# Kernel tuning notes

Measured on AMD Instinct MI355X. Metric: run time of the kernel, lower is better.

## Reference

```python
import jax, jax.numpy as jnp
import numpy as np

N = 20000      # nodes (B in the original code)
T = 8          # timesteps
D_IN = 256     # in_dim (must equal hid_dim due to conv_h_n reuse in original)
D_HID = 256
D_OUT = 64
E = 320000     # edges


def setup_inputs() -> dict:
    key = jax.random.key(0)
    ks = jax.random.split(key, 18)
    s = 0.05
    w = lambda k, shape: jax.random.normal(k, shape, jnp.float32) * s
    return {
        "x": jax.random.normal(ks[0], (N, T, D_IN), jnp.float32),
        "edge_index": jax.random.randint(ks[1], (2, E), 0, N),
        "W_xr": w(ks[2], (D_IN, D_HID)),  "b_xr": w(ks[3], (D_HID,)),
        "W_hr": w(ks[4], (D_HID, D_HID)), "b_hr": w(ks[5], (D_HID,)),
        "W_xz": w(ks[6], (D_IN, D_HID)),  "b_xz": w(ks[7], (D_HID,)),
        "W_hz": w(ks[8], (D_HID, D_HID)), "b_hz": w(ks[9], (D_HID,)),
        "W_hn": w(ks[10], (D_HID, D_HID)), "b_hn": w(ks[11], (D_HID,)),
        "W_fc": w(ks[12], (D_HID, D_OUT)), "b_fc": w(ks[13], (D_OUT,)),
    }


def reference(x, edge_index, W_xr, b_xr, W_hr, b_hr, W_xz, b_xz, W_hz, b_hz,
              W_hn, b_hn, W_fc, b_fc):
    n_nodes = x.shape[0]
    src, dst = edge_index[0], edge_index[1]

    # GCN symmetric normalization with self-loops (PyG GCNConv default):
    # deg[i] = 1 + #incoming edges; norm_e = d^-1/2[src]*d^-1/2[dst]
    deg = jax.ops.segment_sum(jnp.ones(src.shape[0], x.dtype), dst,
                              num_segments=n_nodes) + jnp.asarray(1.0, x.dtype)
    dis = jax.lax.rsqrt(deg)
    enorm = dis[src] * dis[dst]      # [E]
    snorm = dis * dis                # self-loop coefficient 1/deg, [N]

    def gcn(v, W, b):
        vw = v @ W                                              # [N, D]
        agg = jax.ops.segment_sum(vw[src] * enorm[:, None], dst,
                                  num_segments=n_nodes)
        return agg + vw * snorm[:, None] + b

    def step(h, x_t):
        r = jax.nn.sigmoid(gcn(x_t, W_xr, b_xr) + gcn(h, W_hr, b_hr))
        z = jax.nn.sigmoid(gcn(x_t, W_xz, b_xz) + gcn(h, W_hz, b_hz))
        # faithful to original: conv_h_n is applied to BOTH x and h
        n = jnp.tanh(gcn(x_t, W_hn, b_hn) + r * gcn(h, W_hn, b_hn))
        h_new = (1.0 - z) * h + z * n
        return h_new, None

    h0 = jnp.zeros((n_nodes, W_hr.shape[0]), x.dtype)
    h, _ = jax.lax.scan(step, h0, jnp.transpose(x, (1, 0, 2)))  # scan over T
    return h @ W_fc + b_fc
```

## Files before the change

### kernel.cpp

```cpp
#include <hip/hip_runtime.h>
#include <hip/hip_bf16.h>
#include <math.h>

#define N_NODES 20000
#define T_STEPS 8
#define DDIM    256
#define DOUT    64
#define NE      320000
#define XSTR    2048

typedef unsigned short u16;
typedef __attribute__((ext_vector_type(8))) short  short8;
typedef __attribute__((ext_vector_type(4))) float  f32x4;

__device__ __forceinline__ float bf2f(u16 u) {
    union { unsigned int i; float f; } v; v.i = ((unsigned int)u) << 16; return v.f;
}
__device__ __forceinline__ u16 f2bf(float f) {
    union { float f; unsigned int i; } v; v.f = f;
    unsigned int r = v.i + 0x7fff + ((v.i >> 16) & 1);
    return (u16)(r >> 16);
}

__global__ void k_count(const int* __restrict__ dst, int* __restrict__ cnt) {
    int e = blockIdx.x * blockDim.x + threadIdx.x;
    if (e < NE) atomicAdd(&cnt[dst[e]], 1);
}

__global__ void k_degnorm(const int* __restrict__ cnt, float* __restrict__ dis,
                          float* __restrict__ snorm) {
    int n = blockIdx.x * blockDim.x + threadIdx.x;
    if (n < N_NODES) {
        float deg = (float)(cnt[n] + 1);
        dis[n]   = rsqrtf(deg);
        snorm[n] = 1.0f / deg;
    }
}

__global__ void k_scan(const int* __restrict__ cnt, int* __restrict__ rowptr) {
    __shared__ int sums[256];
    const int CH = (N_NODES + 255) / 256;
    int t = threadIdx.x;
    int beg = t * CH;
    int end = beg + CH; if (end > N_NODES) end = N_NODES;
    int s = 0;
    for (int i = beg; i < end; i++) s += cnt[i];
    sums[t] = s;
    __syncthreads();
    if (t == 0) {
        int run = 0;
        for (int i = 0; i < 256; i++) { int v = sums[i]; sums[i] = run; run += v; }
    }
    __syncthreads();
    if (beg < N_NODES) {
        int run = sums[t];
        for (int i = beg; i < end; i++) { rowptr[i] = run; run += cnt[i]; }
        if (end == N_NODES) rowptr[N_NODES] = run;
    }
}

__global__ void k_fill(const int* __restrict__ src, const int* __restrict__ dst,
                       const int* __restrict__ rowptr, int* __restrict__ cursor,
                       const float* __restrict__ dis, int* __restrict__ csr_src,
                       float* __restrict__ csr_norm) {
    int e = blockIdx.x * blockDim.x + threadIdx.x;
    if (e < NE) {
        int d = dst[e], s = src[e];
        int pos = atomicAdd(&cursor[d], 1);
        int i = rowptr[d] + pos;
        if (i < NE) {
            csr_src[i]  = s;
            csr_norm[i] = dis[s] * dis[d];
        }
    }
}

__global__ void k_pack6(const float* __restrict__ Wxr, const float* __restrict__ Wxz,
                        const float* __restrict__ Whn, const float* __restrict__ Whr,
                        const float* __restrict__ Whz, u16* __restrict__ out) {
    int i = blockIdx.x * blockDim.x + threadIdx.x;
    if (i >= 4 * 6 * 64 * 256) return;
    int k    = i & 255;
    int c    = (i >> 8) & 63;
    int tile = (i >> 14) % 6;
    int by   = i / (6 * 64 * 256);
    const float* W;
    switch (tile) {
        case 0: W = Wxr; break; case 1: W = Wxz; break; case 2: W = Whn; break;
        case 3: W = Whr; break; case 4: W = Whz; break; default: W = Whn; break;
    }
    out[i] = f2bf(W[k * DDIM + by * 64 + c]);
}
__global__ void k_packb3(const float* __restrict__ bxr, const float* __restrict__ bhr,
                         const float* __restrict__ bxz, const float* __restrict__ bhz,
                         const float* __restrict__ bhn, float* __restrict__ bout) {
    int c = blockIdx.x * blockDim.x + threadIdx.x;
    if (c < 3 * DDIM) {
        float v;
        if (c < 256)      v = bxr[c] + bhr[c];
        else if (c < 512) v = bxz[c - 256] + bhz[c - 256];
        else              v = bhn[c - 512];
        bout[c] = v;
    }
}

__global__ __launch_bounds__(256) void k_x2bf_all(const float* __restrict__ x,
                                                  u16* __restrict__ out) {
    int i = blockIdx.x * blockDim.x + threadIdx.x;
    if (i >= N_NODES * 512) return;
    size_t o = (size_t)i << 2;
    float4 v = *(const float4*)(x + o);
    ushort4 u; u.x = f2bf(v.x); u.y = f2bf(v.y); u.z = f2bf(v.z); u.w = f2bf(v.w);
    *(ushort4*)(out + o) = u;
}

__global__ __launch_bounds__(256) void k_agg_x(const u16* __restrict__ xall,
                      const int* __restrict__ rowptr, const int* __restrict__ csr_src,
                      const float* __restrict__ csr_norm, const float* __restrict__ snorm,
                      u16* __restrict__ xaall) {
    int n = blockIdx.x * 4 + (threadIdx.x >> 6);
    if (n >= N_NODES) return;
    int lane = threadIdx.x & 63;
    int c4 = lane << 2;
    float sn = snorm[n];
    float acc[8][4];
    const u16* selfp = xall + (size_t)n * XSTR + c4;
#pragma unroll
    for (int t = 0; t < 8; t++) {
        ushort4 v = *(const ushort4*)(selfp + t * DDIM);
        acc[t][0] = bf2f(v.x) * sn; acc[t][1] = bf2f(v.y) * sn;
        acc[t][2] = bf2f(v.z) * sn; acc[t][3] = bf2f(v.w) * sn;
    }
    int beg = rowptr[n], end = rowptr[n + 1];
    int i = beg;
    for (; i + 1 < end; i += 2) {
        const u16* sp0 = xall + (size_t)csr_src[i] * XSTR + c4;
        const u16* sp1 = xall + (size_t)csr_src[i + 1] * XSTR + c4;
        float w0 = csr_norm[i], w1 = csr_norm[i + 1];
        ushort4 g0[8], g1[8];
#pragma unroll
        for (int t = 0; t < 8; t++) g0[t] = *(const ushort4*)(sp0 + t * DDIM);
#pragma unroll
        for (int t = 0; t < 8; t++) g1[t] = *(const ushort4*)(sp1 + t * DDIM);
#pragma unroll
        for (int t = 0; t < 8; t++) {
            acc[t][0] = fmaf(bf2f(g0[t].x), w0, fmaf(bf2f(g1[t].x), w1, acc[t][0]));
            acc[t][1] = fmaf(bf2f(g0[t].y), w0, fmaf(bf2f(g1[t].y), w1, acc[t][1]));
            acc[t][2] = fmaf(bf2f(g0[t].z), w0, fmaf(bf2f(g1[t].z), w1, acc[t][2]));
            acc[t][3] = fmaf(bf2f(g0[t].w), w0, fmaf(bf2f(g1[t].w), w1, acc[t][3]));
        }
    }
    if (i < end) {
        const u16* sp = xall + (size_t)csr_src[i] * XSTR + c4;
        float w = csr_norm[i];
#pragma unroll
        for (int t = 0; t < 8; t++) {
            ushort4 g = *(const ushort4*)(sp + t * DDIM);
            acc[t][0] = fmaf(bf2f(g.x), w, acc[t][0]);
            acc[t][1] = fmaf(bf2f(g.y), w, acc[t][1]);
            acc[t][2] = fmaf(bf2f(g.z), w, acc[t][2]);
            acc[t][3] = fmaf(bf2f(g.w), w, acc[t][3]);
        }
    }
    u16* op = xaall + (size_t)n * XSTR + c4;
#pragma unroll
    for (int t = 0; t < 8; t++) {
        ushort4 o;
        o.x = f2bf(acc[t][0]); o.y = f2bf(acc[t][1]);
        o.z = f2bf(acc[t][2]); o.w = f2bf(acc[t][3]);
        *(ushort4*)(op + t * DDIM) = o;
    }
}

__global__ __launch_bounds__(256) void k_agg_bf(const u16* __restrict__ in,
                      const int* __restrict__ rowptr, const int* __restrict__ csr_src,
                      const float* __restrict__ csr_norm, const float* __restrict__ snorm,
                      u16* __restrict__ out) {
    int n = blockIdx.x * 4 + (threadIdx.x >> 6);
    if (n >= N_NODES) return;
    int lane = threadIdx.x & 63;
    int c4 = lane << 2;
    float sn = snorm[n];
    ushort4 v = *(const ushort4*)(in + (size_t)n * DDIM + c4);
    float a0 = bf2f(v.x) * sn, a1 = bf2f(v.y) * sn, a2 = bf2f(v.z) * sn, a3 = bf2f(v.w) * sn;
    int beg = rowptr[n], end = rowptr[n + 1];
    int i = beg;
    for (; i + 1 < end; i += 2) {
        ushort4 g0 = *(const ushort4*)(in + (size_t)csr_src[i] * DDIM + c4);
        ushort4 g1 = *(const ushort4*)(in + (size_t)csr_src[i + 1] * DDIM + c4);
        float w0 = csr_norm[i], w1 = csr_norm[i + 1];
        a0 = fmaf(bf2f(g0.x), w0, fmaf(bf2f(g1.x), w1, a0));
        a1 = fmaf(bf2f(g0.y), w0, fmaf(bf2f(g1.y), w1, a1));
        a2 = fmaf(bf2f(g0.z), w0, fmaf(bf2f(g1.z), w1, a2));
        a3 = fmaf(bf2f(g0.w), w0, fmaf(bf2f(g1.w), w1, a3));
    }
    if (i < end) {
        ushort4 g = *(const ushort4*)(in + (size_t)csr_src[i] * DDIM + c4);
        float w = csr_norm[i];
        a0 = fmaf(bf2f(g.x), w, a0); a1 = fmaf(bf2f(g.y), w, a1);
        a2 = fmaf(bf2f(g.z), w, a2); a3 = fmaf(bf2f(g.w), w, a3);
    }
    ushort4 o; o.x = f2bf(a0); o.y = f2bf(a1); o.z = f2bf(a2); o.w = f2bf(a3);
    *(ushort4*)(out + (size_t)n * DDIM + c4) = o;
}

__device__ __forceinline__ float sigm(float x) { return 1.0f / (1.0f + expf(-x)); }

__global__ __launch_bounds__(256) void k_gate_gru(const u16* __restrict__ xa, int ldax,
        const u16* __restrict__ ha, const u16* __restrict__ BTpack,
        const float* __restrict__ bias3, float* __restrict__ h, u16* __restrict__ hbf,
        int M) {
    __shared__ u16 Axs[64 * 32];
    __shared__ u16 Ahs[64 * 32];
    __shared__ u16 Bs[6 * 64 * 32];
    int tid = threadIdx.x;
    int w = tid >> 6, lane = tid & 63;
    int rowBase = blockIdx.x * 64;
    int by = blockIdx.y;

    int srow  = lane >> 2;
    int chunk = (lane & 3) ^ ((lane >> 3) & 3);
    int sege  = chunk * 8;
    int arow = rowBase + w * 16 + srow;
    if (arow > M - 1) arow = M - 1;
    size_t xoff = (size_t)arow * ldax + sege;
    size_t hoff = (size_t)arow * DDIM + sege;
    u16* ldsAx = &Axs[w * 16 * 32];
    u16* ldsAh = &Ahs[w * 16 * 32];
    const u16* Bbase = BTpack + (size_t)by * (6 * 64 * 256);

    f32x4 ar[2][2], az[2][2], anx[2][2], anh[2][2];
#pragma unroll
    for (int m = 0; m < 2; m++)
#pragma unroll
        for (int n = 0; n < 2; n++) {
            ar[m][n] = (f32x4){0.f,0.f,0.f,0.f}; az[m][n] = (f32x4){0.f,0.f,0.f,0.f};
            anx[m][n] = (f32x4){0.f,0.f,0.f,0.f}; anh[m][n] = (f32x4){0.f,0.f,0.f,0.f};
        }

    int kq = lane >> 4, lr = lane & 15;
    int kqs = (kq ^ ((lr >> 1) & 3)) << 3;

    for (int k0 = 0; k0 < DDIM; k0 += 32) {
        __builtin_amdgcn_global_load_lds(
            (const __attribute__((address_space(1))) void*)(xa + xoff + k0),
            (__attribute__((address_space(3))) void*)ldsAx, 16, 0, 0);
        __builtin_amdgcn_global_load_lds(
            (const __attribute__((address_space(1))) void*)(ha + hoff + k0),
            (__attribute__((address_space(3))) void*)ldsAh, 16, 0, 0);
#pragma unroll
        for (int j6 = 0; j6 < 6; j6++) {
            int j = w * 6 + j6;
            int tile = j >> 2, q = j & 3;
            const u16* src = Bbase + ((size_t)tile * 64 + q * 16 + srow) * 256 + k0 + sege;
            u16* dst = &Bs[tile * 2048 + q * 512];
            __builtin_amdgcn_global_load_lds(
                (const __attribute__((address_space(1))) void*)src,
                (__attribute__((address_space(3))) void*)dst, 16, 0, 0);
        }
        __syncthreads();

        short8 ax[2], ah[2], bf[6][2];
#pragma unroll
        for (int m = 0; m < 2; m++) {
            int r = (w >> 1) * 32 + m * 16 + lr;
            ax[m] = *(const short8*)&Axs[r * 32 + kqs];
            ah[m] = *(const short8*)&Ahs[r * 32 + kqs];
        }
#pragma unroll
        for (int t = 0; t < 6; t++)
#pragma unroll
            for (int n = 0; n < 2; n++) {
                int c = (w & 1) * 32 + n * 16 + lr;
                bf[t][n] = *(const short8*)&Bs[t * 2048 + c * 32 + kqs];
            }
#pragma unroll
        for (int m = 0; m < 2; m++)
#pragma unroll
            for (int n = 0; n < 2; n++) {
                ar[m][n]  = __builtin_amdgcn_mfma_f32_16x16x32_bf16(ax[m], bf[0][n], ar[m][n], 0, 0, 0);
                ar[m][n]  = __builtin_amdgcn_mfma_f32_16x16x32_bf16(ah[m], bf[3][n], ar[m][n], 0, 0, 0);
                az[m][n]  = __builtin_amdgcn_mfma_f32_16x16x32_bf16(ax[m], bf[1][n], az[m][n], 0, 0, 0);
                az[m][n]  = __builtin_amdgcn_mfma_f32_16x16x32_bf16(ah[m], bf[4][n], az[m][n], 0, 0, 0);
                anx[m][n] = __builtin_amdgcn_mfma_f32_16x16x32_bf16(ax[m], bf[2][n], anx[m][n], 0, 0, 0);
                anh[m][n] = __builtin_amdgcn_mfma_f32_16x16x32_bf16(ah[m], bf[5][n], anh[m][n], 0, 0, 0);
            }
        __syncthreads();
    }

#pragma unroll
    for (int n = 0; n < 2; n++) {
        int col = by * 64 + (w & 1) * 32 + n * 16 + lr;
        float br = bias3[col], bz = bias3[256 + col], bn = bias3[512 + col];
#pragma unroll
        for (int m = 0; m < 2; m++) {
            int row0 = rowBase + (w >> 1) * 32 + m * 16 + kq * 4;
#pragma unroll
            for (int j = 0; j < 4; j++) {
                int row = row0 + j;
                if (row < M) {
                    float r = sigm(ar[m][n][j] + br);
                    float z = sigm(az[m][n][j] + bz);
                    float nn = tanhf(anx[m][n][j] + bn + r * (anh[m][n][j] + bn));
                    size_t idx = (size_t)row * DDIM + col;
                    float hv = h[idx];
                    hv = (1.0f - z) * hv + z * nn;
                    h[idx] = hv;
                    hbf[idx] = f2bf(hv);
                }
            }
        }
    }
}

__global__ __launch_bounds__(256) void k_gemm(const float* __restrict__ A,
        const float* __restrict__ B, const float* __restrict__ bias,
        float* __restrict__ C, int M, int N, int K) {
    __shared__ float Asm[16][132];
    __shared__ float Bsm[16][128];
    int tid = threadIdx.x;
    int tx = tid & 15, ty = tid >> 4;
    int rowBase = blockIdx.x * 128;
    int colBase = blockIdx.y * 128;

    float acc[8][8];
#pragma unroll
    for (int i = 0; i < 8; i++)
#pragma unroll
        for (int j = 0; j < 8; j++) acc[i][j] = 0.0f;

    int arow = tid >> 1;
    int acol = (tid & 1) * 8;
    int brow = tid >> 4;
    int bcol = (tid & 15) * 8;

    bool avalid = (rowBase + arow) < M;
    const float* Aptr = A + (size_t)(rowBase + arow) * K + acol;
    int bc = colBase + bcol;
    bool bvalid = bc < N;

    for (int k0 = 0; k0 < K; k0 += 16) {
        float4 a0 = {0,0,0,0}, a1 = {0,0,0,0};
        if (avalid) {
            a0 = *(const float4*)(Aptr + k0);
            a1 = *(const float4*)(Aptr + k0 + 4);
        }
        Asm[acol + 0][arow] = a0.x; Asm[acol + 1][arow] = a0.y;
        Asm[acol + 2][arow] = a0.z; Asm[acol + 3][arow] = a0.w;
        Asm[acol + 4][arow] = a1.x; Asm[acol + 5][arow] = a1.y;
        Asm[acol + 6][arow] = a1.z; Asm[acol + 7][arow] = a1.w;

        float4 b0 = {0,0,0,0}, b1 = {0,0,0,0};
        if (bvalid) {
            const float* Bp = B + (size_t)(k0 + brow) * N + bc;
            b0 = *(const float4*)(Bp);
            b1 = *(const float4*)(Bp + 4);
        }
        *(float4*)&Bsm[brow][bcol]     = b0;
        *(float4*)&Bsm[brow][bcol + 4] = b1;
        __syncthreads();

#pragma unroll
        for (int k = 0; k < 16; k++) {
            float a[8], b[8];
            *(float4*)&a[0] = *(const float4*)&Asm[k][ty * 8];
            *(float4*)&a[4] = *(const float4*)&Asm[k][ty * 8 + 4];
            *(float4*)&b[0] = *(const float4*)&Bsm[k][tx * 8];
            *(float4*)&b[4] = *(const float4*)&Bsm[k][tx * 8 + 4];
#pragma unroll
            for (int i = 0; i < 8; i++)
#pragma unroll
                for (int j = 0; j < 8; j++)
                    acc[i][j] = fmaf(a[i], b[j], acc[i][j]);
        }
        __syncthreads();
    }

    int c0 = colBase + tx * 8;
    if (c0 < N) {
        float4 bia0 = *(const float4*)(bias + c0);
        float4 bia1 = *(const float4*)(bias + c0 + 4);
#pragma unroll
        for (int i = 0; i < 8; i++) {
            int r = rowBase + ty * 8 + i;
            if (r < M) {
                float4 o0, o1;
                o0.x = acc[i][0] + bia0.x; o0.y = acc[i][1] + bia0.y;
                o0.z = acc[i][2] + bia0.z; o0.w = acc[i][3] + bia0.w;
                o1.x = acc[i][4] + bia1.x; o1.y = acc[i][5] + bia1.y;
                o1.z = acc[i][6] + bia1.z; o1.w = acc[i][7] + bia1.w;
                *(float4*)(C + (size_t)r * N + c0)     = o0;
                *(float4*)(C + (size_t)r * N + c0 + 4) = o1;
            }
        }
    }
}

extern "C" void kernel_launch(void* const* d_in, const int* in_sizes, int n_in,
                              void* d_out, int out_size, void* d_ws, size_t ws_size,
                              hipStream_t stream) {
    const float* x    = (const float*)d_in[0];
    const int*   eidx = (const int*)d_in[1];
    const int*   src  = eidx;
    const int*   dst  = eidx + NE;
    const float* W_xr = (const float*)d_in[2];  const float* b_xr = (const float*)d_in[3];
    const float* W_hr = (const float*)d_in[4];  const float* b_hr = (const float*)d_in[5];
    const float* W_xz = (const float*)d_in[6];  const float* b_xz = (const float*)d_in[7];
    const float* W_hz = (const float*)d_in[8];  const float* b_hz = (const float*)d_in[9];
    const float* W_hn = (const float*)d_in[10]; const float* b_hn = (const float*)d_in[11];
    const float* W_fc = (const float*)d_in[12]; const float* b_fc = (const float*)d_in[13];
    float* out = (float*)d_out;

    char* ws = (char*)d_ws;
    size_t off = 0;
    auto alloc = [&](size_t bytes) -> char* {
        char* p = ws + off;
        off += (bytes + 255) & ~(size_t)255;
        return p;
    };
    const size_t NB  = (size_t)N_NODES * DDIM * 4;
    const size_t NBH = (size_t)N_NODES * DDIM * 2;
    u16*   xall    = (u16*)alloc((size_t)N_NODES * XSTR * 2);
    u16*   xaall   = (u16*)alloc((size_t)N_NODES * XSTR * 2);
    float* h       = (float*)alloc(NB);
    u16*   hbf     = (u16*)alloc(NBH);
    u16*   ha      = (u16*)alloc(NBH);
    u16*   BTpack  = (u16*)alloc((size_t)4 * 6 * 64 * 256 * 2);
    float* bias3   = (float*)alloc(3 * DDIM * 4);
    int*   cnt     = (int*)alloc(N_NODES * 4);
    int*   cursor  = (int*)alloc(N_NODES * 4);
    int*   rowptr  = (int*)alloc((N_NODES + 1) * 4);
    int*   csr_src = (int*)alloc(NE * 4);
    float* csr_nrm = (float*)alloc(NE * 4);
    float* dis     = (float*)alloc(N_NODES * 4);
    float* snorm   = (float*)alloc(N_NODES * 4);

    hipMemsetAsync(cnt, 0, N_NODES * 4, stream);
    hipMemsetAsync(cursor, 0, N_NODES * 4, stream);
    hipMemsetAsync(h, 0, NB, stream);
    hipMemsetAsync(hbf, 0, NBH, stream);

    const int TB = 256;
    k_count<<<(NE + TB - 1) / TB, TB, 0, stream>>>(dst, cnt);
    k_degnorm<<<(N_NODES + TB - 1) / TB, TB, 0, stream>>>(cnt, dis, snorm);
    k_scan<<<1, 256, 0, stream>>>(cnt, rowptr);
    k_fill<<<(NE + TB - 1) / TB, TB, 0, stream>>>(src, dst, rowptr, cursor, dis,
                                                  csr_src, csr_nrm);
    k_pack6<<<(4 * 6 * 64 * 256 + TB - 1) / TB, TB, 0, stream>>>(W_xr, W_xz, W_hn,
                                                                 W_hr, W_hz, BTpack);
    k_packb3<<<(3 * DDIM + TB - 1) / TB, TB, 0, stream>>>(b_xr, b_hr, b_xz, b_hz,
                                                          b_hn, bias3);

    k_x2bf_all<<<(N_NODES * 512 + TB - 1) / TB, TB, 0, stream>>>(x, xall);
    int aggGrid = (N_NODES + 3) / 4;
    k_agg_x<<<aggGrid, TB, 0, stream>>>(xall, rowptr, csr_src, csr_nrm, snorm, xaall);

    dim3 gGate((N_NODES + 63) / 64, 4);
    dim3 gfc((N_NODES + 127) / 128, 1);

    for (int t = 0; t < T_STEPS; t++) {
        k_agg_bf<<<aggGrid, TB, 0, stream>>>(hbf, rowptr, csr_src, csr_nrm, snorm, ha);
        k_gate_gru<<<gGate, TB, 0, stream>>>(xaall + t * DDIM, XSTR, ha, BTpack,
                                             bias3, h, hbf, N_NODES);
    }
    k_gemm<<<gfc, TB, 0, stream>>>(h, W_fc, b_fc, out, N_NODES, DOUT, DDIM);
}
```

Measured before the change: 1.216 ms.

## Widen aggregation loads, use grid-stride loops, and double gate GEMM row tile

The x-aggregation kernel now gives each half-wave four timesteps and loads 16-byte vectors, unrolling over four edges per iteration. Both aggregation kernels switch to persistent grid-stride loops over a fixed 2048-block grid, with four-edge unrolling for more memory-level parallelism. The gate GEMM tile grows from 64 to 128 rows per block so each loaded weight tile is reused across more rows. The cost is more accumulator registers and more LDS in the gate kernel, which may lower occupancy.

```diff
diff --git a/kernel.cpp b/kernel.cpp
--- a/kernel.cpp
+++ b/kernel.cpp
@@ -11,6 +11,7 @@
 
 typedef unsigned short u16;
 typedef __attribute__((ext_vector_type(8))) short  short8;
+typedef __attribute__((ext_vector_type(8))) unsigned short ushort8;
 typedef __attribute__((ext_vector_type(4))) float  f32x4;
 
 __device__ __forceinline__ float bf2f(u16 u) {
@@ -114,61 +115,71 @@
     *(ushort4*)(out + o) = u;
 }
 
+#define XLOAD(G, sp) \
+    ushort8 G##0 = *(const ushort8*)((sp));        \
+    ushort8 G##1 = *(const ushort8*)((sp) + 256);  \
+    ushort8 G##2 = *(const ushort8*)((sp) + 512);  \
+    ushort8 G##3 = *(const ushort8*)((sp) + 768);
+#define XACC(G, W) {                                        \
+    _Pragma("unroll")                                       \
+    for (int q = 0; q < 8; q++) {                           \
+        acc0[q] = fmaf(bf2f(G##0[q]), (W), acc0[q]);        \
+        acc1[q] = fmaf(bf2f(G##1[q]), (W), acc1[q]);        \
+        acc2[q] = fmaf(bf2f(G##2[q]), (W), acc2[q]);        \
+        acc3[q] = fmaf(bf2f(G##3[q]), (W), acc3[q]);        \
+    } }
+
 __global__ __launch_bounds__(256) void k_agg_x(const u16* __restrict__ xall,
                       const int* __restrict__ rowptr, const int* __restrict__ csr_src,
                       const float* __restrict__ csr_norm, const float* __restrict__ snorm,
                       u16* __restrict__ xaall) {
-    int n = blockIdx.x * 4 + (threadIdx.x >> 6);
-    if (n >= N_NODES) return;
     int lane = threadIdx.x & 63;
-    int c4 = lane << 2;
-    float sn = snorm[n];
-    float acc[8][4];
-    const u16* selfp = xall + (size_t)n * XSTR + c4;
-#pragma unroll
-    for (int t = 0; t < 8; t++) {
-        ushort4 v = *(const ushort4*)(selfp + t * DDIM);
-        acc[t][0] = bf2f(v.x) * sn; acc[t][1] = bf2f(v.y) * sn;
-        acc[t][2] = bf2f(v.z) * sn; acc[t][3] = bf2f(v.w) * sn;
-    }
-    int beg = rowptr[n], end = rowptr[n + 1];
-    int i = beg;
-    for (; i + 1 < end; i += 2) {
-        const u16* sp0 = xall + (size_t)csr_src[i] * XSTR + c4;
-        const u16* sp1 = xall + (size_t)csr_src[i + 1] * XSTR + c4;
-        float w0 = csr_norm[i], w1 = csr_norm[i + 1];
-        ushort4 g0[8], g1[8];
-#pragma unroll
-        for (int t = 0; t < 8; t++) g0[t] = *(const ushort4*)(sp0 + t * DDIM);
-#pragma unroll
-        for (int t = 0; t < 8; t++) g1[t] = *(const ushort4*)(sp1 + t * DDIM);
-#pragma unroll
-        for (int t = 0; t < 8; t++) {
-            acc[t][0] = fmaf(bf2f(g0[t].x), w0, fmaf(bf2f(g1[t].x), w1, acc[t][0]));
-            acc[t][1] = fmaf(bf2f(g0[t].y), w0, fmaf(bf2f(g1[t].y), w1, acc[t][1]));
-            acc[t][2] = fmaf(bf2f(g0[t].z), w0, fmaf(bf2f(g1[t].z), w1, acc[t][2]));
-            acc[t][3] = fmaf(bf2f(g0[t].w), w0, fmaf(bf2f(g1[t].w), w1, acc[t][3]));
-        }
-    }
-    if (i < end) {
-        const u16* sp = xall + (size_t)csr_src[i] * XSTR + c4;
-        float w = csr_norm[i];
-#pragma unroll
-        for (int t = 0; t < 8; t++) {
-            ushort4 g = *(const ushort4*)(sp + t * DDIM);
-            acc[t][0] = fmaf(bf2f(g.x), w, acc[t][0]);
-            acc[t][1] = fmaf(bf2f(g.y), w, acc[t][1]);
-            acc[t][2] = fmaf(bf2f(g.z), w, acc[t][2]);
-            acc[t][3] = fmaf(bf2f(g.w), w, acc[t][3]);
-        }
-    }
-    u16* op = xaall + (size_t)n * XSTR + c4;
-#pragma unroll
-    for (int t = 0; t < 8; t++) {
-        ushort4 o;
-        o.x = f2bf(acc[t][0]); o.y = f2bf(acc[t][1]);
-        o.z = f2bf(acc[t][2]); o.w = f2bf(acc[t][3]);
-        *(ushort4*)(op + t * DDIM) = o;
+    int th   = lane >> 5;
+    int c8   = (lane & 31) << 3;
+    int off  = th * 1024 + c8;
+    int wid  = blockIdx.x * 4 + (threadIdx.x >> 6);
+    int nw   = gridDim.x * 4;
+    for (int n = wid; n < N_NODES; n += nw) {
+        float sn = snorm[n];
+        const u16* selfp = xall + (size_t)n * XSTR + off;
+        float acc0[8], acc1[8], acc2[8], acc3[8];
+        {
+            XLOAD(s, selfp)
+#pragma unroll
+            for (int q = 0; q < 8; q++) {
+                acc0[q] = bf2f(s0[q]) * sn; acc1[q] = bf2f(s1[q]) * sn;
+                acc2[q] = bf2f(s2[q]) * sn; acc3[q] = bf2f(s3[q]) * sn;
+            }
+        }
+        int beg = rowptr[n], end = rowptr[n + 1];
+        int i = beg;
+        for (; i + 3 < end; i += 4) {
+            const u16* spA = xall + (size_t)csr_src[i]     * XSTR + off;
+            const u16* spB = xall + (size_t)csr_src[i + 1] * XSTR + off;
+            const u16* spC = xall + (size_t)csr_src[i + 2] * XSTR + off;
+            const u16* spD = xall + (size_t)csr_src[i + 3] * XSTR + off;
+            float wA = csr_norm[i], wB = csr_norm[i + 1];
+            float wC = csr_norm[i + 2], wD = csr_norm[i + 3];
+            XLOAD(a, spA) XLOAD(b, spB) XLOAD(c, spC) XLOAD(d, spD)
+            XACC(a, wA) XACC(b, wB) XACC(c, wC) XACC(d, wD)
+        }
+        for (; i < end; i++) {
+            const u16* sp = xall + (size_t)csr_src[i] * XSTR + off;
+            float w = csr_norm[i];
+            XLOAD(a, sp)
+            XACC(a, w)
+        }
+        u16* op = xaall + (size_t)n * XSTR + off;
+        ushort8 o0, o1, o2, o3;
+#pragma unroll
+        for (int q = 0; q < 8; q++) {
+            o0[q] = f2bf(acc0[q]); o1[q] = f2bf(acc1[q]);
+            o2[q] = f2bf(acc2[q]); o3[q] = f2bf(acc3[q]);
+        }
+        *(ushort8*)(op)       = o0;
+        *(ushort8*)(op + 256) = o1;
+        *(ushort8*)(op + 512) = o2;
+        *(ushort8*)(op + 768) = o3;
     }
 }
 
@@ -176,32 +187,42 @@
                       const int* __restrict__ rowptr, const int* __restrict__ csr_src,
                       const float* __restrict__ csr_norm, const float* __restrict__ snorm,
                       u16* __restrict__ out) {
-    int n = blockIdx.x * 4 + (threadIdx.x >> 6);
-    if (n >= N_NODES) return;
     int lane = threadIdx.x & 63;
     int c4 = lane << 2;
-    float sn = snorm[n];
-    ushort4 v = *(const ushort4*)(in + (size_t)n * DDIM + c4);
-    float a0 = bf2f(v.x) * sn, a1 = bf2f(v.y) * sn, a2 = bf2f(v.z) * sn, a3 = bf2f(v.w) * sn;
-    int beg = rowptr[n], end = rowptr[n + 1];
-    int i = beg;
-    for (; i + 1 < end; i += 2) {
-        ushort4 g0 = *(const ushort4*)(in + (size_t)csr_src[i] * DDIM + c4);
-        ushort4 g1 = *(const ushort4*)(in + (size_t)csr_src[i + 1] * DDIM + c4);
-        float w0 = csr_norm[i], w1 = csr_norm[i + 1];
-        a0 = fmaf(bf2f(g0.x), w0, fmaf(bf2f(g1.x), w1, a0));
-        a1 = fmaf(bf2f(g0.y), w0, fmaf(bf2f(g1.y), w1, a1));
-        a2 = fmaf(bf2f(g0.z), w0, fmaf(bf2f(g1.z), w1, a2));
-        a3 = fmaf(bf2f(g0.w), w0, fmaf(bf2f(g1.w), w1, a3));
-    }
-    if (i < end) {
-        ushort4 g = *(const ushort4*)(in + (size_t)csr_src[i] * DDIM + c4);
-        float w = csr_norm[i];
-        a0 = fmaf(bf2f(g.x), w, a0); a1 = fmaf(bf2f(g.y), w, a1);
-        a2 = fmaf(bf2f(g.z), w, a2); a3 = fmaf(bf2f(g.w), w, a3);
-    }
-    ushort4 o; o.x = f2bf(a0); o.y = f2bf(a1); o.z = f2bf(a2); o.w = f2bf(a3);
-    *(ushort4*)(out + (size_t)n * DDIM + c4) = o;
+    int wid = blockIdx.x * 4 + (threadIdx.x >> 6);
+    int nw  = gridDim.x * 4;
+    for (int n = wid; n < N_NODES; n += nw) {
+        float sn = snorm[n];
+        ushort4 v = *(const ushort4*)(in + (size_t)n * DDIM + c4);
+        float a0 = bf2f(v.x) * sn, a1 = bf2f(v.y) * sn;
+        float a2 = bf2f(v.z) * sn, a3 = bf2f(v.w) * sn;
+        int beg = rowptr[n], end = rowptr[n + 1];
+        int i = beg;
+        for (; i + 3 < end; i += 4) {
+            ushort4 gA = *(const ushort4*)(in + (size_t)csr_src[i]     * DDIM + c4);
+            ushort4 gB = *(const ushort4*)(in + (size_t)csr_src[i + 1] * DDIM + c4);
+            ushort4 gC = *(const ushort4*)(in + (size_t)csr_src[i + 2] * DDIM + c4);
+            ushort4 gD = *(const ushort4*)(in + (size_t)csr_src[i + 3] * DDIM + c4);
+            float wA = csr_norm[i], wB = csr_norm[i + 1];
+            float wC = csr_norm[i + 2], wD = csr_norm[i + 3];
+            a0 = fmaf(bf2f(gA.x), wA, a0); a1 = fmaf(bf2f(gA.y), wA, a1);
+            a2 = fmaf(bf2f(gA.z), wA, a2); a3 = fmaf(bf2f(gA.w), wA, a3);
+            a0 = fmaf(bf2f(gB.x), wB, a0); a1 = fmaf(bf2f(gB.y), wB, a1);
+            a2 = fmaf(bf2f(gB.z), wB, a2); a3 = fmaf(bf2f(gB.w), wB, a3);
+            a0 = fmaf(bf2f(gC.x), wC, a0); a1 = fmaf(bf2f(gC.y), wC, a1);
+            a2 = fmaf(bf2f(gC.z), wC, a2); a3 = fmaf(bf2f(gC.w), wC, a3);
+            a0 = fmaf(bf2f(gD.x), wD, a0); a1 = fmaf(bf2f(gD.y), wD, a1);
+            a2 = fmaf(bf2f(gD.z), wD, a2); a3 = fmaf(bf2f(gD.w), wD, a3);
+        }
+        for (; i < end; i++) {
+            ushort4 g = *(const ushort4*)(in + (size_t)csr_src[i] * DDIM + c4);
+            float w = csr_norm[i];
+            a0 = fmaf(bf2f(g.x), w, a0); a1 = fmaf(bf2f(g.y), w, a1);
+            a2 = fmaf(bf2f(g.z), w, a2); a3 = fmaf(bf2f(g.w), w, a3);
+        }
+        ushort4 o; o.x = f2bf(a0); o.y = f2bf(a1); o.z = f2bf(a2); o.w = f2bf(a3);
+        *(ushort4*)(out + (size_t)n * DDIM + c4) = o;
+    }
 }
 
 __device__ __forceinline__ float sigm(float x) { return 1.0f / (1.0f + expf(-x)); }
@@ -210,28 +231,35 @@
         const u16* __restrict__ ha, const u16* __restrict__ BTpack,
         const float* __restrict__ bias3, float* __restrict__ h, u16* __restrict__ hbf,
         int M) {
-    __shared__ u16 Axs[64 * 32];
-    __shared__ u16 Ahs[64 * 32];
+    __shared__ u16 Axs[128 * 32];
+    __shared__ u16 Ahs[128 * 32];
     __shared__ u16 Bs[6 * 64 * 32];
     int tid = threadIdx.x;
     int w = tid >> 6, lane = tid & 63;
-    int rowBase = blockIdx.x * 64;
+    int wr = w >> 1, wcol = w & 1;
+    int rowBase = blockIdx.x * 128;
     int by = blockIdx.y;
 
     int srow  = lane >> 2;
     int chunk = (lane & 3) ^ ((lane >> 3) & 3);
     int sege  = chunk * 8;
-    int arow = rowBase + w * 16 + srow;
-    if (arow > M - 1) arow = M - 1;
-    size_t xoff = (size_t)arow * ldax + sege;
-    size_t hoff = (size_t)arow * DDIM + sege;
-    u16* ldsAx = &Axs[w * 16 * 32];
-    u16* ldsAh = &Ahs[w * 16 * 32];
+    int arow0 = rowBase + w * 16 + srow;
+    int arow1 = arow0 + 64;
+    if (arow0 > M - 1) arow0 = M - 1;
+    if (arow1 > M - 1) arow1 = M - 1;
+    size_t xoff0 = (size_t)arow0 * ldax + sege;
+    size_t xoff1 = (size_t)arow1 * ldax + sege;
+    size_t hoff0 = (size_t)arow0 * DDIM + sege;
+    size_t hoff1 = (size_t)arow1 * DDIM + sege;
+    u16* ldsAx0 = &Axs[w * 512];
+    u16* ldsAx1 = &Axs[2048 + w * 512];
+    u16* ldsAh0 = &Ahs[w * 512];
+    u16* ldsAh1 = &Ahs[2048 + w * 512];
     const u16* Bbase = BTpack + (size_t)by * (6 * 64 * 256);
 
-    f32x4 ar[2][2], az[2][2], anx[2][2], anh[2][2];
-#pragma unroll
-    for (int m = 0; m < 2; m++)
+    f32x4 ar[4][2], az[4][2], anx[4][2], anh[4][2];
+#pragma unroll
+    for (int m = 0; m < 4; m++)
 #pragma unroll
         for (int n = 0; n < 2; n++) {
             ar[m][n] = (f32x4){0.f,0.f,0.f,0.f}; az[m][n] = (f32x4){0.f,0.f,0.f,0.f};
@@ -243,58 +271,62 @@
 
     for (int k0 = 0; k0 < DDIM; k0 += 32) {
         __builtin_amdgcn_global_load_lds(
-            (const __attribute__((address_space(1))) void*)(xa + xoff + k0),
-            (__attribute__((address_space(3))) void*)ldsAx, 16, 0, 0);
+            (const __attribute__((address_space(1))) void*)(xa + xoff0 + k0),
+            (__attribute__((address_space(3))) void*)ldsAx0, 16, 0, 0);
         __builtin_amdgcn_global_load_lds(
-            (const __attribute__((address_space(1))) void*)(ha + hoff + k0),
-            (__attribute__((address_space(3))) void*)ldsAh, 16, 0, 0);
-#pragma unroll
-        for (int j6 = 0; j6 < 6; j6++) {
-            int j = w * 6 + j6;
-            int tile = j >> 2, q = j & 3;
-            const u16* src = Bbase + ((size_t)tile * 64 + q * 16 + srow) * 256 + k0 + sege;
-            u16* dst = &Bs[tile * 2048 + q * 512];
+            (const __attribute__((address_space(1))) void*)(xa + xoff1 + k0),
+            (__attribute__((address_space(3))) void*)ldsAx1, 16, 0, 0);
+        __builtin_amdgcn_global_load_lds(
+            (const __attribute__((address_space(1))) void*)(ha + hoff0 + k0),
+            (__attribute__((address_space(3))) void*)ldsAh0, 16, 0, 0);
+        __builtin_amdgcn_global_load_lds(
+            (const __attribute__((address_space(1))) void*)(ha + hoff1 + k0),
+            (__attribute__((address_space(3))) void*)ldsAh1, 16, 0, 0);
+#pragma unroll
+        for (int j = 0; j < 6; j++) {
+            const u16* srcp = Bbase + ((size_t)j * 64 + w * 16 + srow) * 256 + k0 + sege;
+            u16* dstp = &Bs[j * 2048 + w * 512];
             __builtin_amdgcn_global_load_lds(
-                (const __attribute__((address_space(1))) void*)src,
-                (__attribute__((address_space(3))) void*)dst, 16, 0, 0);
+                (const __attribute__((address_space(1))) void*)srcp,
+                (__attribute__((address_space(3))) void*)dstp, 16, 0, 0);
         }
         __syncthreads();
 
-        short8 ax[2], ah[2], bf[6][2];
-#pragma unroll
-        for (int m = 0; m < 2; m++) {
-            int r = (w >> 1) * 32 + m * 16 + lr;
-            ax[m] = *(const short8*)&Axs[r * 32 + kqs];
-            ah[m] = *(const short8*)&Ahs[r * 32 + kqs];
+        short8 axf[4], ahf[4], bf[6][2];
+#pragma unroll
+        for (int m = 0; m < 4; m++) {
+            int r = wr * 64 + m * 16 + lr;
+            axf[m] = *(const short8*)&Axs[r * 32 + kqs];
+            ahf[m] = *(const short8*)&Ahs[r * 32 + kqs];
         }
 #pragma unroll
         for (int t = 0; t < 6; t++)
 #pragma unroll
             for (int n = 0; n < 2; n++) {
-                int c = (w & 1) * 32 + n * 16 + lr;
+                int c = wcol * 32 + n * 16 + lr;
                 bf[t][n] = *(const short8*)&Bs[t * 2048 + c * 32 + kqs];
             }
 #pragma unroll
-        for (int m = 0; m < 2; m++)
+        for (int m = 0; m < 4; m++)
 #pragma unroll
             for (int n = 0; n < 2; n++) {
-                ar[m][n]  = __builtin_amdgcn_mfma_f32_16x16x32_bf16(ax[m], bf[0][n], ar[m][n], 0, 0, 0);
-                ar[m][n]  = __builtin_amdgcn_mfma_f32_16x16x32_bf16(ah[m], bf[3][n], ar[m][n], 0, 0, 0);
-                az[m][n]  = __builtin_amdgcn_mfma_f32_16x16x32_bf16(ax[m], bf[1][n], az[m][n], 0, 0, 0);
-                az[m][n]  = __builtin_amdgcn_mfma_f32_16x16x32_bf16(ah[m], bf[4][n], az[m][n], 0, 0, 0);
-                anx[m][n] = __builtin_amdgcn_mfma_f32_16x16x32_bf16(ax[m], bf[2][n], anx[m][n], 0, 0, 0);
-                anh[m][n] = __builtin_amdgcn_mfma_f32_16x16x32_bf16(ah[m], bf[5][n], anh[m][n], 0, 0, 0);
+                ar[m][n]  = __builtin_amdgcn_mfma_f32_16x16x32_bf16(axf[m], bf[0][n], ar[m][n], 0, 0, 0);
+                ar[m][n]  = __builtin_amdgcn_mfma_f32_16x16x32_bf16(ahf[m], bf[3][n], ar[m][n], 0, 0, 0);
+                az[m][n]  = __builtin_amdgcn_mfma_f32_16x16x32_bf16(axf[m], bf[1][n], az[m][n], 0, 0, 0);
+                az[m][n]  = __builtin_amdgcn_mfma_f32_16x16x32_bf16(ahf[m], bf[4][n], az[m][n], 0, 0, 0);
+                anx[m][n] = __builtin_amdgcn_mfma_f32_16x16x32_bf16(axf[m], bf[2][n], anx[m][n], 0, 0, 0);
+                anh[m][n] = __builtin_amdgcn_mfma_f32_16x16x32_bf16(ahf[m], bf[5][n], anh[m][n], 0, 0, 0);
             }
         __syncthreads();
     }
 
 #pragma unroll
     for (int n = 0; n < 2; n++) {
-        int col = by * 64 + (w & 1) * 32 + n * 16 + lr;
+        int col = by * 64 + wcol * 32 + n * 16 + lr;
         float br = bias3[col], bz = bias3[256 + col], bn = bias3[512 + col];
 #pragma unroll
-        for (int m = 0; m < 2; m++) {
-            int row0 = rowBase + (w >> 1) * 32 + m * 16 + kq * 4;
+        for (int m = 0; m < 4; m++) {
+            int row0 = rowBase + wr * 64 + m * 16 + kq * 4;
 #pragma unroll
             for (int j = 0; j < 4; j++) {
                 int row = row0 + j;
@@ -452,14 +484,13 @@
                                                           b_hn, bias3);
 
     k_x2bf_all<<<(N_NODES * 512 + TB - 1) / TB, TB, 0, stream>>>(x, xall);
-    int aggGrid = (N_NODES + 3) / 4;
-    k_agg_x<<<aggGrid, TB, 0, stream>>>(xall, rowptr, csr_src, csr_nrm, snorm, xaall);
-
-    dim3 gGate((N_NODES + 63) / 64, 4);
+    k_agg_x<<<2048, TB, 0, stream>>>(xall, rowptr, csr_src, csr_nrm, snorm, xaall);
+
+    dim3 gGate((N_NODES + 127) / 128, 4);
     dim3 gfc((N_NODES + 127) / 128, 1);
 
     for (int t = 0; t < T_STEPS; t++) {
-        k_agg_bf<<<aggGrid, TB, 0, stream>>>(hbf, rowptr, csr_src, csr_nrm, snorm, ha);
+        k_agg_bf<<<2048, TB, 0, stream>>>(hbf, rowptr, csr_src, csr_nrm, snorm, ha);
         k_gate_gru<<<gGate, TB, 0, stream>>>(xaall + t * DDIM, XSTR, ha, BTpack,
                                              bias3, h, hbf, N_NODES);
     }
```

Result: slower. 1.264 ms (+4.0%).
